# Performance work log

Hardware: AMD Instinct MI355X
Metric: run time of the kernel (lower is better)

The kernel has to match this reference:

```python
import jax, jax.numpy as jnp
import numpy as np

B, T, D_MODEL, D_STATE = 8, 2048, 1024, 256


def setup_inputs() -> dict:
    key = jax.random.key(0)
    ks = jax.random.split(key, 11)
    def lecun(k, shape):
        fan_in = shape[0]
        return jax.random.normal(k, shape, jnp.float32) / jnp.sqrt(jnp.float32(fan_in))
    return {
        "x": jax.random.normal(ks[0], (B, T, D_MODEL), jnp.float32),
        "W_in": lecun(ks[1], (D_MODEL, D_STATE)),
        "b_in": jnp.zeros((D_STATE,), jnp.float32),
        "W_gate": lecun(ks[2], (D_MODEL, D_MODEL)),
        "b_gate": jnp.zeros((D_MODEL,), jnp.float32),
        "A": lecun(ks[3], (D_STATE, D_STATE)),
        "Bm": lecun(ks[4], (D_STATE, D_STATE)),
        "C": lecun(ks[5], (D_MODEL, D_STATE)),
        "D": lecun(ks[6], (D_MODEL, D_STATE)),
        "W_out": lecun(ks[7], (D_MODEL, D_MODEL)),
        "b_out": jnp.zeros((D_MODEL,), jnp.float32),
    }


def reference(x, W_in, b_in, W_gate, b_gate, A, Bm, C, D, W_out, b_out):
    b, t, d_model = x.shape
    d_state = A.shape[0]
    u = x @ W_in + b_in                      # [B,T,d_state]
    g = jax.nn.sigmoid(x @ W_gate + b_gate)  # [B,T,d_model]

    u_seq = jnp.swapaxes(u, 0, 1)  # [T,B,d_state]
    g_seq = jnp.swapaxes(g, 0, 1)  # [T,B,d_model]
    x_seq = jnp.swapaxes(x, 0, 1)  # [T,B,d_model]

    def step(h_prev, inputs):
        u_t, g_t, x_t = inputs
        h_t = jnp.tanh(h_prev @ A + u_t @ Bm)            # [B,d_state]
        y_t = h_t @ C.T + u_t @ D.T                      # [B,d_model]
        y_t = g_t * y_t + (1.0 - g_t) * x_t
        return h_t, y_t

    h0 = jnp.zeros((b, d_state), x.dtype)
    _, ys = jax.lax.scan(step, h0, xs=(u_seq, g_seq, x_seq))
    ys = jnp.swapaxes(ys, 0, 1)  # [B,T,d_model]
    return ys @ W_out + b_out + x
```

## Files before the change

### kernel.cpp

```cpp
#include <hip/hip_runtime.h>
#include <math.h>


enum { E_NONE = 0, E_BIASBF = 1, E_SIGBF = 2, E_ACC = 3, E_BIASRES = 4, E_CVTBF = 5 };

typedef __attribute__((ext_vector_type(8))) short bf16x8;
typedef __attribute__((ext_vector_type(4))) float f32x4;

static __device__ inline unsigned short f2bf(float f) {
    unsigned u = __builtin_bit_cast(unsigned, f);
    unsigned r = (u + 0x7fff + ((u >> 16) & 1)) >> 16;
    return (unsigned short)r;
}
static __device__ inline unsigned pack2(float a, float b) {
    return (unsigned)f2bf(a) | ((unsigned)f2bf(b) << 16);
}
static __device__ inline float bflo(unsigned u) {
    return __builtin_bit_cast(float, u << 16);
}
static __device__ inline float bfhi(unsigned u) {
    return __builtin_bit_cast(float, u & 0xffff0000u);
}
static __device__ inline float tanh_fast(float x) {
    float e = __builtin_amdgcn_exp2f(x * 2.8853900817779268f);
    float t = __builtin_amdgcn_rcpf(e + 1.0f);
    return fmaf(-2.0f, t, 1.0f);
}

__global__ __launch_bounds__(256) void cvt_bf(
    const float* __restrict__ in, unsigned short* __restrict__ out, int n8)
{
    int i = blockIdx.x * 256 + threadIdx.x;
    if (i >= n8) return;
    float4 a = ((const float4*)in)[i * 2];
    float4 b = ((const float4*)in)[i * 2 + 1];
    uint4 o;
    o.x = pack2(a.x, a.y); o.y = pack2(a.z, a.w);
    o.z = pack2(b.x, b.y); o.w = pack2(b.z, b.w);
    ((uint4*)out)[i] = o;
}

__global__ __launch_bounds__(256) void transpose_bf(
    const float* __restrict__ in, unsigned short* __restrict__ out, int R, int C)
{
    __shared__ float tile[32][33];
    const int bx = blockIdx.x * 32, by = blockIdx.y * 32;
    const int tx = threadIdx.x & 31, ty = threadIdx.x >> 5;
#pragma unroll
    for (int i = 0; i < 32; i += 8)
        tile[ty + i][tx] = in[(size_t)(by + ty + i) * C + bx + tx];
    __syncthreads();
#pragma unroll
    for (int i = 0; i < 32; i += 8)
        out[(size_t)(bx + ty + i) * R + by + tx] = f2bf(tile[tx][ty + i]);
}

template <int EPI>
__global__ __launch_bounds__(256) void gemm_mfma(
    const unsigned short* __restrict__ Ag,
    const unsigned short* __restrict__ Bg,
    const float* __restrict__ bias, const float* __restrict__ res,
    void* Cg, int M, int N, int K)
{
    __shared__ __align__(16) unsigned char Lds[2][32768];
    const int tid = threadIdx.x;
    const int w = tid >> 6, l = tid & 63;
    const int r = l & 15, g = l >> 4;
    const int m0 = blockIdx.y * 128, n0 = blockIdx.x * 128;

    const unsigned char* agp[4];
    const unsigned char* bgp[4];
#pragma unroll
    for (int j = 0; j < 4; ++j) {
        const int c = w * 256 + j * 64 + l;
        const int row = c >> 3;
        const unsigned offp = ((unsigned)(c & 7) * 16u) ^ ((unsigned)(row & 7) * 16u);
        agp[j] = (const unsigned char*)Ag + ((size_t)(m0 + row) * K) * 2 + offp;
        bgp[j] = (const unsigned char*)Bg + ((size_t)(n0 + row) * K) * 2 + offp;
    }

#define STAGE(BUF)                                                            \
    {                                                                         \
      _Pragma("unroll")                                                       \
      for (int j = 0; j < 4; ++j) {                                           \
        __builtin_amdgcn_global_load_lds(                                     \
            (const __attribute__((address_space(1))) unsigned*)(agp[j]),      \
            (__attribute__((address_space(3))) unsigned*)&Lds[(BUF)][w * 4096 + j * 1024], \
            16, 0, 0);                                                        \
        __builtin_amdgcn_global_load_lds(                                     \
            (const __attribute__((address_space(1))) unsigned*)(bgp[j]),      \
            (__attribute__((address_space(3))) unsigned*)&Lds[(BUF)][16384 + w * 4096 + j * 1024], \
            16, 0, 0);                                                        \
        agp[j] += 128; bgp[j] += 128;                                         \
      }                                                                       \
    }

    f32x4 acc[2][8];
#pragma unroll
    for (int mt = 0; mt < 2; ++mt)
#pragma unroll
        for (int nt = 0; nt < 8; ++nt) acc[mt][nt] = (f32x4){0.f, 0.f, 0.f, 0.f};

    const int nk = K >> 6;
    STAGE(0)
    __syncthreads();
    for (int t = 0; t < nk; ++t) {
        const int buf = t & 1;
        if (t + 1 < nk) { STAGE(buf ^ 1) }
        bf16x8 af[2][2], bf[8][2];
#pragma unroll
        for (int s = 0; s < 2; ++s) {
#pragma unroll
            for (int mt = 0; mt < 2; ++mt) {
                const int row = w * 32 + mt * 16 + r;
                af[mt][s] = *(const bf16x8*)&Lds[buf][row * 128 +
                    ((s * 64 + 16 * g) ^ (16 * (row & 7)))];
            }
#pragma unroll
            for (int nt = 0; nt < 8; ++nt) {
                const int row = nt * 16 + r;
                bf[nt][s] = *(const bf16x8*)&Lds[buf][16384 + row * 128 +
                    ((s * 64 + 16 * g) ^ (16 * (row & 7)))];
            }
        }
#pragma unroll
        for (int s = 0; s < 2; ++s)
#pragma unroll
            for (int mt = 0; mt < 2; ++mt)
#pragma unroll
                for (int nt = 0; nt < 8; ++nt)
                    acc[mt][nt] = __builtin_amdgcn_mfma_f32_16x16x32_bf16(
                        af[mt][s], bf[nt][s], acc[mt][nt], 0, 0, 0);
        __syncthreads();
    }
#undef STAGE

#pragma unroll
    for (int mt = 0; mt < 2; ++mt)
#pragma unroll
        for (int nt = 0; nt < 8; ++nt) {
            const int n = n0 + nt * 16 + r;
            float bv = 0.f;
            if (EPI == E_BIASBF || EPI == E_SIGBF || EPI == E_BIASRES) bv = bias[n];
#pragma unroll
            for (int q = 0; q < 4; ++q) {
                const int m = m0 + w * 32 + mt * 16 + g * 4 + q;
                const size_t idx = (size_t)m * N + n;
                float v = acc[mt][nt][q] + bv;
                if (EPI == E_SIGBF) v = 1.f / (1.f + expf(-v));
                if (EPI == E_ACC) v += ((const float*)Cg)[idx];
                if (EPI == E_BIASRES) v += res[idx];
                if (EPI == E_BIASBF || EPI == E_SIGBF || EPI == E_CVTBF)
                    ((unsigned short*)Cg)[idx] = f2bf(v);
                else
                    ((float*)Cg)[idx] = v;
            }
        }
}

__global__ __launch_bounds__(256, 1) void scan_mfma(
    const float* __restrict__ Amat, const unsigned short* __restrict__ u2bf,
    unsigned short* __restrict__ hbf)
{
    constexpr int T = 2048;
    __shared__ __align__(16) unsigned char LDSM[64 * 1024 + 2 * 32 * 1024];
    unsigned char* Hb = LDSM;
    unsigned char* Ub = LDSM + 65536;

    const int tid = threadIdx.x;
    const int w = tid >> 6, l = tid & 63;
    const int r = l & 15, g = l >> 4, r8 = r & 7;
    const int qb = (r >> 3) << 1;
    const int m0 = w * 64;

    for (int i = tid; i < 1024; i += 256) ((unsigned*)Hb)[i] = 0u;

    bf16x8 af[4][8];
#pragma unroll
    for (int mt = 0; mt < 4; ++mt) {
        const int m = m0 + mt * 16 + r;
#pragma unroll
        for (int kt = 0; kt < 8; ++kt) {
            unsigned wd[4];
#pragma unroll
            for (int jw = 0; jw < 4; ++jw) {
                const int k = kt * 32 + g * 8 + jw * 2;
                wd[jw] = pack2(Amat[(size_t)k * 256 + m],
                               Amat[(size_t)(k + 1) * 256 + m]);
            }
            af[mt][kt] = __builtin_bit_cast(bf16x8, *(uint4*)wd);
        }
    }

    unsigned uoff[4];
#pragma unroll
    for (int mt = 0; mt < 4; ++mt) {
        const int state = m0 + mt * 16 + g * 4 + qb;
        const int gran = state >> 3;
        uoff[mt] = (unsigned)(r8 * 512 + ((gran ^ r8) * 16) + ((state & 7) * 2));
    }

    const unsigned char* usrc[8];
#pragma unroll
    for (int j = 0; j < 8; ++j) {
        const int flat = j * 256 + tid;
        const int ri = flat >> 5, s = ri >> 3, b = ri & 7, gp = flat & 31;
        usrc[j] = (const unsigned char*)u2bf + ((size_t)(b * T + s) * 512)
                + (unsigned)((gp ^ b) * 16);
    }

#pragma unroll
    for (int j = 0; j < 8; ++j) {
        __builtin_amdgcn_global_load_lds(
            (const __attribute__((address_space(1))) unsigned*)(usrc[j]),
            (__attribute__((address_space(3))) unsigned*)(Ub + (j * 256 + tid) * 16),
            16, 0, 0);
        usrc[j] += 4096;
    }
    asm volatile("s_waitcnt vmcnt(0) lgkmcnt(0)" ::: "memory");
    __builtin_amdgcn_sched_barrier(0);
    __builtin_amdgcn_s_barrier();
    __builtin_amdgcn_sched_barrier(0);

#define SCAN_STEP(I)                                                          \
  {                                                                           \
    const int tt = t0 + (I);                                                  \
    const unsigned br_ = ((unsigned)tt & 15u) * 4096u;                        \
    const unsigned bw_ = ((unsigned)(tt + 1) & 15u) * 4096u;                  \
    bf16x8 hf[8];                                                             \
    _Pragma("unroll")                                                         \
    for (int kt = 0; kt < 8; ++kt)                                            \
      hf[kt] = *(const bf16x8*)(Hb + br_ +                                    \
                                (unsigned)(kt * 32 + g * 8 + r8) * 16u);      \
    unsigned uval[4];                                                         \
    _Pragma("unroll")                                                         \
    for (int mt = 0; mt < 4; ++mt)                                            \
      uval[mt] = *(const unsigned*)(Ub + ubuf_ + (unsigned)(I) * 4096u +      \
                                    uoff[mt]);                                \
    asm volatile("s_waitcnt lgkmcnt(0)" ::: "memory");                        \
    __builtin_amdgcn_sched_barrier(0);                                        \
    f32x4 p0[4], p1[4];                                                       \
    _Pragma("unroll")                                                         \
    for (int mt = 0; mt < 4; ++mt) {                                          \
      p0[mt] = (f32x4){0.f, 0.f, 0.f, 0.f};                                   \
      p1[mt] = (f32x4){0.f, 0.f, 0.f, 0.f};                                   \
    }                                                                         \
    _Pragma("unroll")                                                         \
    for (int kt = 0; kt < 4; ++kt) {                                          \
      _Pragma("unroll")                                                       \
      for (int mt = 0; mt < 4; ++mt) {                                        \
        p0[mt] = __builtin_amdgcn_mfma_f32_16x16x32_bf16(af[mt][kt], hf[kt],  \
                                                         p0[mt], 0, 0, 0);    \
        p1[mt] = __builtin_amdgcn_mfma_f32_16x16x32_bf16(                     \
            af[mt][kt + 4], hf[kt + 4], p1[mt], 0, 0, 0);                     \
      }                                                                       \
    }                                                                         \
    _Pragma("unroll")                                                         \
    for (int mt = 0; mt < 4; ++mt) {                                          \
      const int mb = m0 + mt * 16 + g * 4;                                    \
      float s0 = p0[mt][qb] + p1[mt][qb] + bflo(uval[mt]);                    \
      float s1 = p0[mt][qb + 1] + p1[mt][qb + 1] + bfhi(uval[mt]);            \
      float h0 = tanh_fast(s0), h1 = tanh_fast(s1);                           \
      unsigned pk;                                                            \
      asm("v_cvt_pk_bf16_f32 %0, %1, %2" : "=v"(pk) : "v"(h0), "v"(h1));      \
      *(unsigned*)(Hb + bw_ +                                                 \
          (unsigned)((mb >> 5) * 32 + ((mb >> 3) & 3) * 8 + r8) * 16u +       \
          (unsigned)(((mb & 7) + qb) * 2)) = pk;                              \
    }                                                                         \
    if ((I) == 7 && t0 > 0) {                                                 \
      _Pragma("unroll")                                                       \
      for (int cc = 0; cc < 8; ++cc) {                                        \
        const unsigned bd_ = (unsigned)((t0 - 7 + cc) & 15) * 4096u;          \
        uint4 dat = *(const uint4*)(Hb + bd_ + (unsigned)tid * 16u);          \
        const int kt_ = tid >> 5, sl_ = tid & 31;                             \
        const size_t off = ((size_t)((sl_ & 7) * T + (t0 - 8 + cc)) * 256 +   \
                            kt_ * 32 + (sl_ >> 3) * 8);                       \
        *(uint4*)(hbf + off) = dat;                                           \
      }                                                                       \
    }                                                                         \
    asm volatile("s_waitcnt lgkmcnt(0)" ::: "memory");                        \
    __builtin_amdgcn_sched_barrier(0);                                        \
    if ((I) == 7) {                                                           \
      asm volatile("s_waitcnt vmcnt(8)" ::: "memory");                        \
      __builtin_amdgcn_sched_barrier(0);                                      \
    }                                                                         \
    __builtin_amdgcn_s_barrier();                                             \
    __builtin_amdgcn_sched_barrier(0);                                        \
  }

    for (int t0 = 0; t0 < T; t0 += 8) {
        const unsigned ubuf_ = (unsigned)((t0 >> 3) & 1) * 32768u;
        if (t0 + 8 < T) {
            const unsigned nb_ = ubuf_ ^ 32768u;
#pragma unroll
            for (int j = 0; j < 8; ++j) {
                __builtin_amdgcn_global_load_lds(
                    (const __attribute__((address_space(1))) unsigned*)(usrc[j]),
                    (__attribute__((address_space(3))) unsigned*)(Ub + nb_ + (j * 256 + tid) * 16),
                    16, 0, 0);
                usrc[j] += 4096;
            }
        }
        SCAN_STEP(0)
        SCAN_STEP(1)
        SCAN_STEP(2)
        SCAN_STEP(3)
        SCAN_STEP(4)
        SCAN_STEP(5)
        SCAN_STEP(6)
        SCAN_STEP(7)
    }
#undef SCAN_STEP

    {
#pragma unroll
        for (int cc = 0; cc < 8; ++cc) {
            const unsigned bd_ = (unsigned)((T - 7 + cc) & 15) * 4096u;
            uint4 dat = *(const uint4*)(Hb + bd_ + (unsigned)tid * 16u);
            const int kt_ = tid >> 5, sl_ = tid & 31;
            const size_t off = ((size_t)((sl_ & 7) * T + (T - 8 + cc)) * 256 +
                                kt_ * 32 + (sl_ >> 3) * 8);
            *(uint4*)(hbf + off) = dat;
        }
    }
}

__global__ __launch_bounds__(256) void ewise(
    const unsigned short* __restrict__ g8, const float* __restrict__ big,
    const float* __restrict__ x, unsigned short* __restrict__ ys, int n8)
{
    int i = blockIdx.x * 256 + threadIdx.x;
    if (i >= n8) return;
    uint4 gv = ((const uint4*)g8)[i];
    float4 b0 = ((const float4*)big)[i * 2], b1 = ((const float4*)big)[i * 2 + 1];
    float4 x0 = ((const float4*)x)[i * 2], x1 = ((const float4*)x)[i * 2 + 1];
    float gg[8] = {bflo(gv.x), bfhi(gv.x), bflo(gv.y), bfhi(gv.y),
                   bflo(gv.z), bfhi(gv.z), bflo(gv.w), bfhi(gv.w)};
    float bb[8] = {b0.x, b0.y, b0.z, b0.w, b1.x, b1.y, b1.z, b1.w};
    float xx[8] = {x0.x, x0.y, x0.z, x0.w, x1.x, x1.y, x1.z, x1.w};
    float yy[8];
#pragma unroll
    for (int k = 0; k < 8; ++k) yy[k] = gg[k] * bb[k] + (1.f - gg[k]) * xx[k];
    uint4 o;
    o.x = pack2(yy[0], yy[1]); o.y = pack2(yy[2], yy[3]);
    o.z = pack2(yy[4], yy[5]); o.w = pack2(yy[6], yy[7]);
    ((uint4*)ys)[i] = o;
}

extern "C" void kernel_launch(void* const* d_in, const int* in_sizes, int n_in,
                              void* d_out, int out_size, void* d_ws, size_t ws_size,
                              hipStream_t stream)
{
    const float* x      = (const float*)d_in[0];
    const float* W_in   = (const float*)d_in[1];
    const float* b_in   = (const float*)d_in[2];
    const float* W_gate = (const float*)d_in[3];
    const float* b_gate = (const float*)d_in[4];
    const float* Amat   = (const float*)d_in[5];
    const float* Bm     = (const float*)d_in[6];
    const float* Cm     = (const float*)d_in[7];
    const float* Dm     = (const float*)d_in[8];
    const float* W_out  = (const float*)d_in[9];
    const float* b_out  = (const float*)d_in[10];

    const int T = 2048, DM = 1024, DS = 256;
    const int M = 8 * T;
    const size_t MB = 1024 * 1024;
    char* ws = (char*)d_ws;

    unsigned short* xbf  = (unsigned short*)(ws);
    unsigned short* ysbf = xbf;
    unsigned short* u    = (unsigned short*)(ws + 32 * MB);
    unsigned short* u2   = (unsigned short*)(ws + 40 * MB);
    unsigned short* h    = (unsigned short*)(ws + 56 * MB);
    unsigned short* WinT = (unsigned short*)(ws + 64 * MB);
    unsigned short* BmT  = (unsigned short*)(ws + 64 * MB + 512 * 1024);
    unsigned short* WgT  = (unsigned short*)(ws + 65 * MB);
    unsigned short* WoT  = (unsigned short*)(ws + 67 * MB);
    unsigned short* Cbf  = (unsigned short*)(ws + 69 * MB);
    unsigned short* Dbf  = (unsigned short*)(ws + 69 * MB + 512 * 1024);
    float*          big  = (float*)(ws + 70 * MB);
    unsigned short* gbf  = (unsigned short*)(ws + 134 * MB);

    cvt_bf<<<M * DM / 8 / 256, 256, 0, stream>>>(x, xbf, M * DM / 8);
    transpose_bf<<<dim3(DS / 32, DM / 32), 256, 0, stream>>>(W_in, WinT, DM, DS);
    transpose_bf<<<dim3(DS / 32, DS / 32), 256, 0, stream>>>(Bm, BmT, DS, DS);
    transpose_bf<<<dim3(DM / 32, DM / 32), 256, 0, stream>>>(W_gate, WgT, DM, DM);
    transpose_bf<<<dim3(DM / 32, DM / 32), 256, 0, stream>>>(W_out, WoT, DM, DM);
    cvt_bf<<<DM * DS / 8 / 256, 256, 0, stream>>>(Cm, Cbf, DM * DS / 8);
    cvt_bf<<<DM * DS / 8 / 256, 256, 0, stream>>>(Dm, Dbf, DM * DS / 8);

    gemm_mfma<E_BIASBF><<<dim3(DS / 128, M / 128), 256, 0, stream>>>(
        xbf, WinT, b_in, nullptr, u, M, DS, DM);
    gemm_mfma<E_NONE><<<dim3(DM / 128, M / 128), 256, 0, stream>>>(
        u, Dbf, nullptr, nullptr, big, M, DM, DS);
    gemm_mfma<E_CVTBF><<<dim3(DS / 128, M / 128), 256, 0, stream>>>(
        u, BmT, nullptr, nullptr, u2, M, DS, DS);
    gemm_mfma<E_SIGBF><<<dim3(DM / 128, M / 128), 256, 0, stream>>>(
        xbf, WgT, b_gate, nullptr, gbf, M, DM, DM);
    scan_mfma<<<1, 256, 0, stream>>>(Amat, u2, h);
    gemm_mfma<E_ACC><<<dim3(DM / 128, M / 128), 256, 0, stream>>>(
        h, Cbf, nullptr, nullptr, big, M, DM, DS);
    ewise<<<M * DM / 8 / 256, 256, 0, stream>>>(gbf, big, x, ysbf, M * DM / 8);
    gemm_mfma<E_BIASRES><<<dim3(DM / 128, M / 128), 256, 0, stream>>>(
        ysbf, WoT, b_out, x, (float*)d_out, M, DM, DM);
}
```

Before: 1.700 ms.

## Split recurrent scan across batch: one workgroup per batch element

```diff
diff --git a/kernel.cpp b/kernel.cpp
--- a/kernel.cpp
+++ b/kernel.cpp
@@ -107,7 +107,7 @@
     for (int t = 0; t < nk; ++t) {
         const int buf = t & 1;
         if (t + 1 < nk) { STAGE(buf ^ 1) }
-        bf16x8 af[2][2], bf[8][2];
+        bf16x8 af[2][2], bfr[8][2];
 #pragma unroll
         for (int s = 0; s < 2; ++s) {
 #pragma unroll
@@ -119,7 +119,7 @@
 #pragma unroll
             for (int nt = 0; nt < 8; ++nt) {
                 const int row = nt * 16 + r;
-                bf[nt][s] = *(const bf16x8*)&Lds[buf][16384 + row * 128 +
+                bfr[nt][s] = *(const bf16x8*)&Lds[buf][16384 + row * 128 +
                     ((s * 64 + 16 * g) ^ (16 * (row & 7)))];
             }
         }
@@ -130,7 +130,7 @@
 #pragma unroll
                 for (int nt = 0; nt < 8; ++nt)
                     acc[mt][nt] = __builtin_amdgcn_mfma_f32_16x16x32_bf16(
-                        af[mt][s], bf[nt][s], acc[mt][nt], 0, 0, 0);
+                        af[mt][s], bfr[nt][s], acc[mt][nt], 0, 0, 0);
         __syncthreads();
     }
 #undef STAGE
@@ -163,17 +163,19 @@
     unsigned short* __restrict__ hbf)
 {
     constexpr int T = 2048;
-    __shared__ __align__(16) unsigned char LDSM[64 * 1024 + 2 * 32 * 1024];
+    constexpr int NCH = T / 8;
+    __shared__ __align__(16) unsigned char LDSM[8192 + 2 * 4096];
     unsigned char* Hb = LDSM;
-    unsigned char* Ub = LDSM + 65536;
+    unsigned char* Ub = LDSM + 8192;
 
     const int tid = threadIdx.x;
+    const int bb = blockIdx.x;
     const int w = tid >> 6, l = tid & 63;
-    const int r = l & 15, g = l >> 4, r8 = r & 7;
-    const int qb = (r >> 3) << 1;
+    const int r = l & 15, g = l >> 4;
     const int m0 = w * 64;
-
-    for (int i = tid; i < 1024; i += 256) ((unsigned*)Hb)[i] = 0u;
+    const bool c1 = (r & 1) != 0, c2 = (r & 2) != 0;
+
+    if (tid < 128) ((unsigned*)Hb)[tid] = 0u;
 
     bf16x8 af[4][8];
 #pragma unroll
@@ -192,31 +194,15 @@
         }
     }
 
-    unsigned uoff[4];
-#pragma unroll
-    for (int mt = 0; mt < 4; ++mt) {
-        const int state = m0 + mt * 16 + g * 4 + qb;
-        const int gran = state >> 3;
-        uoff[mt] = (unsigned)(r8 * 512 + ((gran ^ r8) * 16) + ((state & 7) * 2));
-    }
-
-    const unsigned char* usrc[8];
-#pragma unroll
-    for (int j = 0; j < 8; ++j) {
-        const int flat = j * 256 + tid;
-        const int ri = flat >> 5, s = ri >> 3, b = ri & 7, gp = flat & 31;
-        usrc[j] = (const unsigned char*)u2bf + ((size_t)(b * T + s) * 512)
-                + (unsigned)((gp ^ b) * 16);
-    }
-
-#pragma unroll
-    for (int j = 0; j < 8; ++j) {
-        __builtin_amdgcn_global_load_lds(
-            (const __attribute__((address_space(1))) unsigned*)(usrc[j]),
-            (__attribute__((address_space(3))) unsigned*)(Ub + (j * 256 + tid) * 16),
-            16, 0, 0);
-        usrc[j] += 4096;
-    }
+    const unsigned char* u2b = (const unsigned char*)u2bf + (size_t)bb * T * 512;
+    unsigned short* hb = hbf + (size_t)bb * T * 256;
+
+    __builtin_amdgcn_global_load_lds(
+        (const __attribute__((address_space(1))) unsigned*)(u2b + tid * 16),
+        (__attribute__((address_space(3))) unsigned*)(Ub + tid * 16), 16, 0, 0);
+    __builtin_amdgcn_global_load_lds(
+        (const __attribute__((address_space(1))) unsigned*)(u2b + 4096 + tid * 16),
+        (__attribute__((address_space(3))) unsigned*)(Ub + 4096 + tid * 16), 16, 0, 0);
     asm volatile("s_waitcnt vmcnt(0) lgkmcnt(0)" ::: "memory");
     __builtin_amdgcn_sched_barrier(0);
     __builtin_amdgcn_s_barrier();
@@ -224,19 +210,18 @@
 
 #define SCAN_STEP(I)                                                          \
   {                                                                           \
-    const int tt = t0 + (I);                                                  \
-    const unsigned br_ = ((unsigned)tt & 15u) * 4096u;                        \
-    const unsigned bw_ = ((unsigned)(tt + 1) & 15u) * 4096u;                  \
     bf16x8 hf[8];                                                             \
     _Pragma("unroll")                                                         \
     for (int kt = 0; kt < 8; ++kt)                                            \
-      hf[kt] = *(const bf16x8*)(Hb + br_ +                                    \
-                                (unsigned)(kt * 32 + g * 8 + r8) * 16u);      \
-    unsigned uval[4];                                                         \
-    _Pragma("unroll")                                                         \
-    for (int mt = 0; mt < 4; ++mt)                                            \
-      uval[mt] = *(const unsigned*)(Ub + ubuf_ + (unsigned)(I) * 4096u +      \
-                                    uoff[mt]);                                \
+      hf[kt] = *(const bf16x8*)(Hb + c15 + (I) * 512u +                       \
+                                (unsigned)(kt * 64 + g * 16));                \
+    float uu[4];                                                              \
+    _Pragma("unroll")                                                         \
+    for (int mt = 0; mt < 4; ++mt) {                                          \
+      unsigned short us = *(const unsigned short*)(                           \
+          Uc + (I) * 512u + (unsigned)((m0 + mt * 16 + g * 4 + (r & 3)) * 2));\
+      uu[mt] = bflo(us);                                                      \
+    }                                                                         \
     asm volatile("s_waitcnt lgkmcnt(0)" ::: "memory");                        \
     __builtin_amdgcn_sched_barrier(0);                                        \
     f32x4 p0[4], p1[4];                                                       \
@@ -255,52 +240,32 @@
             af[mt][kt + 4], hf[kt + 4], p1[mt], 0, 0, 0);                     \
       }                                                                       \
     }                                                                         \
+    const unsigned bwb = ((I) == 7) ? (c15 ^ 4096u) : (c15 + ((I) + 1) * 512u);\
     _Pragma("unroll")                                                         \
     for (int mt = 0; mt < 4; ++mt) {                                          \
-      const int mb = m0 + mt * 16 + g * 4;                                    \
-      float s0 = p0[mt][qb] + p1[mt][qb] + bflo(uval[mt]);                    \
-      float s1 = p0[mt][qb + 1] + p1[mt][qb + 1] + bfhi(uval[mt]);            \
-      float h0 = tanh_fast(s0), h1 = tanh_fast(s1);                           \
+      float s0 = p0[mt][0] + p1[mt][0];                                       \
+      float s1 = p0[mt][1] + p1[mt][1];                                       \
+      float s2 = p0[mt][2] + p1[mt][2];                                       \
+      float s3 = p0[mt][3] + p1[mt][3];                                       \
+      float sv = c2 ? (c1 ? s3 : s2) : (c1 ? s1 : s0);                        \
+      float hv = tanh_fast(sv + uu[mt]);                                      \
       unsigned pk;                                                            \
-      asm("v_cvt_pk_bf16_f32 %0, %1, %2" : "=v"(pk) : "v"(h0), "v"(h1));      \
-      *(unsigned*)(Hb + bw_ +                                                 \
-          (unsigned)((mb >> 5) * 32 + ((mb >> 3) & 3) * 8 + r8) * 16u +       \
-          (unsigned)(((mb & 7) + qb) * 2)) = pk;                              \
-    }                                                                         \
-    if ((I) == 7 && t0 > 0) {                                                 \
-      _Pragma("unroll")                                                       \
-      for (int cc = 0; cc < 8; ++cc) {                                        \
-        const unsigned bd_ = (unsigned)((t0 - 7 + cc) & 15) * 4096u;          \
-        uint4 dat = *(const uint4*)(Hb + bd_ + (unsigned)tid * 16u);          \
-        const int kt_ = tid >> 5, sl_ = tid & 31;                             \
-        const size_t off = ((size_t)((sl_ & 7) * T + (t0 - 8 + cc)) * 256 +   \
-                            kt_ * 32 + (sl_ >> 3) * 8);                       \
-        *(uint4*)(hbf + off) = dat;                                           \
-      }                                                                       \
+      asm("v_cvt_pk_bf16_f32 %0, %1, %2" : "=v"(pk) : "v"(hv), "v"(hv));      \
+      if (r < 4)                                                              \
+        *(unsigned short*)(Hb + bwb +                                         \
+            (unsigned)((m0 + mt * 16 + g * 4 + r) * 2)) = (unsigned short)pk; \
     }                                                                         \
     asm volatile("s_waitcnt lgkmcnt(0)" ::: "memory");                        \
     __builtin_amdgcn_sched_barrier(0);                                        \
-    if ((I) == 7) {                                                           \
-      asm volatile("s_waitcnt vmcnt(8)" ::: "memory");                        \
-      __builtin_amdgcn_sched_barrier(0);                                      \
-    }                                                                         \
     __builtin_amdgcn_s_barrier();                                             \
     __builtin_amdgcn_sched_barrier(0);                                        \
   }
 
-    for (int t0 = 0; t0 < T; t0 += 8) {
-        const unsigned ubuf_ = (unsigned)((t0 >> 3) & 1) * 32768u;
-        if (t0 + 8 < T) {
-            const unsigned nb_ = ubuf_ ^ 32768u;
-#pragma unroll
-            for (int j = 0; j < 8; ++j) {
-                __builtin_amdgcn_global_load_lds(
-                    (const __attribute__((address_space(1))) unsigned*)(usrc[j]),
-                    (__attribute__((address_space(3))) unsigned*)(Ub + nb_ + (j * 256 + tid) * 16),
-                    16, 0, 0);
-                usrc[j] += 4096;
-            }
-        }
+    for (int chunk = 0; chunk < NCH; ++chunk) {
+        const int t0 = chunk * 8;
+        const unsigned c15 = (unsigned)(t0 & 15) * 512u;
+        unsigned char* Uc = Ub + ((unsigned)(chunk & 1) << 12);
+
         SCAN_STEP(0)
         SCAN_STEP(1)
         SCAN_STEP(2)
@@ -309,20 +274,29 @@
         SCAN_STEP(5)
         SCAN_STEP(6)
         SCAN_STEP(7)
+
+        {
+            const int flat = tid * 16;
+            const int i = flat >> 9, byte = flat & 511;
+            const int slot = (t0 + 1 + i) & 15;
+            uint4 dat = *(const uint4*)(Hb + slot * 512 + byte);
+            *(uint4*)((unsigned char*)hb + (size_t)(t0 + i) * 512 + byte) = dat;
+        }
+        if (chunk + 2 < NCH) {
+            __builtin_amdgcn_global_load_lds(
+                (const __attribute__((address_space(1))) unsigned*)(
+                    u2b + (size_t)(t0 + 16) * 512 + tid * 16),
+                (__attribute__((address_space(3))) unsigned*)(
+                    Ub + ((unsigned)(chunk & 1) << 12) + tid * 16), 16, 0, 0);
+            asm volatile("s_waitcnt vmcnt(2)" ::: "memory");
+        } else {
+            asm volatile("s_waitcnt vmcnt(1)" ::: "memory");
+        }
+        __builtin_amdgcn_sched_barrier(0);
+        __builtin_amdgcn_s_barrier();
+        __builtin_amdgcn_sched_barrier(0);
     }
 #undef SCAN_STEP
-
-    {
-#pragma unroll
-        for (int cc = 0; cc < 8; ++cc) {
-            const unsigned bd_ = (unsigned)((T - 7 + cc) & 15) * 4096u;
-            uint4 dat = *(const uint4*)(Hb + bd_ + (unsigned)tid * 16u);
-            const int kt_ = tid >> 5, sl_ = tid & 31;
-            const size_t off = ((size_t)((sl_ & 7) * T + (T - 8 + cc)) * 256 +
-                                kt_ * 32 + (sl_ >> 3) * 8);
-            *(uint4*)(hbf + off) = dat;
-        }
-    }
 }
 
 __global__ __launch_bounds__(256) void ewise(
@@ -398,7 +372,7 @@
         u, BmT, nullptr, nullptr, u2, M, DS, DS);
     gemm_mfma<E_SIGBF><<<dim3(DM / 128, M / 128), 256, 0, stream>>>(
         xbf, WgT, b_gate, nullptr, gbf, M, DM, DM);
-    scan_mfma<<<1, 256, 0, stream>>>(Amat, u2, h);
+    scan_mfma<<<8, 256, 0, stream>>>(Amat, u2, h);
     gemm_mfma<E_ACC><<<dim3(DM / 128, M / 128), 256, 0, stream>>>(
         h, Cbf, nullptr, nullptr, big, M, DM, DS);
     ewise<<<M * DM / 8 / 256, 256, 0, stream>>>(gbf, big, x, ysbf, M * DM / 8);
```

Result: faster. 1.559 ms (-8.3%).
